# Kernel optimization log

Measured on AMD Instinct MI355X. Metric: run time of the kernel, lower is better.

Reference implementation:

```python
import jax, jax.numpy as jnp
import numpy as np

H_HEADS = 8
HIDDEN = 512
D_K = HIDDEN // H_HEADS


def setup_inputs() -> dict:
    key = jax.random.key(0)
    ks = jax.random.split(key, 16)
    B, T = 4, 1024
    P = 2 * T - 1
    s = 0.02
    inp = {
        "x": jax.random.normal(ks[0], (B, T, HIDDEN), dtype=jnp.float32),
        "pos_emb": jax.random.normal(ks[1], (1, P, HIDDEN), dtype=jnp.float32),
        "Wq": jax.random.normal(ks[2], (HIDDEN, HIDDEN), dtype=jnp.float32) * s,
        "bq": jnp.zeros((HIDDEN,), dtype=jnp.float32),
        "Wk": jax.random.normal(ks[3], (HIDDEN, HIDDEN), dtype=jnp.float32) * s,
        "bk": jnp.zeros((HIDDEN,), dtype=jnp.float32),
        "Wv": jax.random.normal(ks[4], (HIDDEN, HIDDEN), dtype=jnp.float32) * s,
        "bv": jnp.zeros((HIDDEN,), dtype=jnp.float32),
        "Wp": jax.random.normal(ks[5], (HIDDEN, HIDDEN), dtype=jnp.float32) * s,
        "bp": jnp.zeros((HIDDEN,), dtype=jnp.float32),
        "Wo": jax.random.normal(ks[6], (HIDDEN, HIDDEN), dtype=jnp.float32) * s,
        "bo": jnp.zeros((HIDDEN,), dtype=jnp.float32),
        "pos_bias_u": jax.random.normal(ks[7], (H_HEADS, D_K), dtype=jnp.float32) * s,
        "pos_bias_v": jax.random.normal(ks[8], (H_HEADS, D_K), dtype=jnp.float32) * s,
    }
    return inp


def rel_shift(x):
    # x: (B, H, T, P). Transformer-XL relative shift.
    B, H, T, P = x.shape
    x = jnp.pad(x, ((0, 0), (0, 0), (0, 0), (1, 0)))  # (B,H,T,P+1)
    x = x.reshape(B, H, P + 1, T)[:, :, 1:, :]          # drop first row
    return x.reshape(B, H, T, P)


def reference(x, pos_emb, Wq, bq, Wk, bk, Wv, bv, Wp, bp, Wo, bo, pos_bias_u, pos_bias_v):
    B, T, _ = x.shape
    Hh, d = H_HEADS, D_K
    scale = 1.0 / jnp.sqrt(jnp.asarray(d, dtype=x.dtype))

    q = (x @ Wq + bq).reshape(B, T, Hh, d)                       # (B,T,H,d)
    k = (x @ Wk + bk).reshape(B, T, Hh, d).transpose(0, 2, 1, 3)  # (B,H,T,d)
    v = (x @ Wv + bv).reshape(B, T, Hh, d).transpose(0, 2, 1, 3)  # (B,H,T,d)
    P = pos_emb.shape[1]
    p = (pos_emb @ Wp + bp).reshape(pos_emb.shape[0], P, Hh, d).transpose(0, 2, 1, 3)  # (1,H,P,d)

    q_u = (q + pos_bias_u).transpose(0, 2, 1, 3)  # (B,H,T,d)
    q_v = (q + pos_bias_v).transpose(0, 2, 1, 3)  # (B,H,T,d)

    # content-position term with rel-shift (broadcast over batch dim of p)
    matrix_bd = jnp.matmul(q_v, p.transpose(0, 1, 3, 2))  # (B,H,T,P)
    matrix_bd = rel_shift(matrix_bd)[:, :, :, :T] * scale  # (B,H,T,T)

    # content-content term + additive bias, scaled softmax
    scores = jnp.matmul(q_u, k.transpose(0, 1, 3, 2)) * scale + matrix_bd
    attn = jax.nn.softmax(scores.astype(jnp.float32), axis=-1).astype(x.dtype)
    out = jnp.matmul(attn, v)                 # (B,H,T,d)
    out = out.transpose(0, 2, 1, 3).reshape(B, T, Hh * d)
    return out @ Wo + bo
```

## Files before the change

kernel.cpp:

```cpp
#include <hip/hip_runtime.h>
#include <math.h>

#define BATCH 4
#define SEQ   1024
#define HID   512
#define NHEAD 8

typedef unsigned short u16;
typedef unsigned int   u32;
typedef short  short8 __attribute__((ext_vector_type(8)));
typedef float  f32x4  __attribute__((ext_vector_type(4)));

__device__ __forceinline__ u16 f2bf(float x) {
  u32 u = __builtin_bit_cast(u32, x);
  u32 r = (u + 0x7FFFu + ((u >> 16) & 1u)) >> 16;
  return (u16)r;
}

#define DPPMAX(x, ctrl)                                                        \
  x = fmaxf(x, __builtin_bit_cast(float, __builtin_amdgcn_update_dpp(          \
                   0, __builtin_bit_cast(int, x), ctrl, 0xf, 0xf, true)))

__global__ __launch_bounds__(256)
void cvt_two(const float* __restrict__ x, const float* __restrict__ pe,
             u16* __restrict__ xb, u16* __restrict__ peb) {
  int i = blockIdx.x * 256 + threadIdx.x;
  const float* s;
  u16* d;
  if (i < 524288) {
    s = x; d = xb;
  } else {
    i -= 524288;
    if (i >= 262016) return;
    s = pe; d = peb;
  }
  float4 v = *(const float4*)&s[(size_t)i * 4];
  ushort4 o;
  o.x = f2bf(v.x); o.y = f2bf(v.y); o.z = f2bf(v.z); o.w = f2bf(v.w);
  *(ushort4*)&d[(size_t)i * 4] = o;
}

__global__ __launch_bounds__(256)
void transpose_w(const float* w0, const float* w1, const float* w2,
                 const float* w3, const float* w4, u16* __restrict__ wt) {
  const float* src;
  switch (blockIdx.z) {
    case 0: src = w0; break;
    case 1: src = w1; break;
    case 2: src = w2; break;
    case 3: src = w3; break;
    default: src = w4; break;
  }
  u16* dst = wt + (size_t)blockIdx.z * 512 * 512;
  __shared__ float t[32][33];
  const int tx = threadIdx.x, ty = threadIdx.y;
  const int k0 = blockIdx.x * 32, n0 = blockIdx.y * 32;
#pragma unroll
  for (int r = 0; r < 4; ++r)
    t[ty + 8 * r][tx] = src[(size_t)(k0 + ty + 8 * r) * 512 + n0 + tx];
  __syncthreads();
#pragma unroll
  for (int r = 0; r < 4; ++r)
    dst[(size_t)(n0 + ty + 8 * r) * 512 + k0 + tx] = f2bf(t[tx][ty + 8 * r]);
}

template <int MF, int NF>
__device__ __forceinline__ void gemm_core(const u16* __restrict__ A,
                                          const u16* __restrict__ Bt,
                                          int m0, int n0, u16* As, u16* Bs,
                                          f32x4 (&acc)[MF][NF]) {
  const int tid = threadIdx.x;
  const int wid = tid >> 6, lane = tid & 63;
  const int lr = lane & 15, lg = lane >> 4;
  const int wm = wid >> 1, wn = wid & 1;
  const int srow = tid >> 3, sc = tid & 7;
#pragma unroll
  for (int i = 0; i < MF; ++i)
#pragma unroll
    for (int j = 0; j < NF; ++j) acc[i][j] = (f32x4)0.f;

  for (int kt = 0; kt < 8; ++kt) {
    const int k0 = kt * 64;
    short8 la[MF], lb[NF];
#pragma unroll
    for (int r = 0; r < MF; ++r)
      la[r] = *(const short8*)&A[(size_t)(m0 + srow + 32 * r) * 512 + k0 + sc * 8];
#pragma unroll
    for (int r = 0; r < NF; ++r)
      lb[r] = *(const short8*)&Bt[(size_t)(n0 + srow + 32 * r) * 512 + k0 + sc * 8];
    __syncthreads();
#pragma unroll
    for (int r = 0; r < MF; ++r) {
      int row = srow + 32 * r;
      *(short8*)&As[row * 64 + ((sc ^ (row & 7)) * 8)] = la[r];
    }
#pragma unroll
    for (int r = 0; r < NF; ++r) {
      int row = srow + 32 * r;
      *(short8*)&Bs[row * 64 + ((sc ^ (row & 7)) * 8)] = lb[r];
    }
    __syncthreads();
#pragma unroll
    for (int kc = 0; kc < 2; ++kc) {
      const int ch = kc * 4 + lg;
      short8 af[MF], bfr[NF];
#pragma unroll
      for (int mt = 0; mt < MF; ++mt) {
        int row = wm * (MF * 16) + mt * 16 + lr;
        af[mt] = *(const short8*)&As[row * 64 + ((ch ^ (row & 7)) * 8)];
      }
#pragma unroll
      for (int nt = 0; nt < NF; ++nt) {
        int row = wn * (NF * 16) + nt * 16 + lr;
        bfr[nt] = *(const short8*)&Bs[row * 64 + ((ch ^ (row & 7)) * 8)];
      }
#pragma unroll
      for (int mt = 0; mt < MF; ++mt)
#pragma unroll
        for (int nt = 0; nt < NF; ++nt)
          acc[mt][nt] = __builtin_amdgcn_mfma_f32_16x16x32_bf16(
              af[mt], bfr[nt], acc[mt][nt], 0, 0, 0);
    }
  }
}

__global__ __launch_bounds__(256)
void gemm_qkvp(const u16* __restrict__ xbf, const u16* __restrict__ pebf,
               const u16* __restrict__ wt,
               const float* __restrict__ bq, const float* __restrict__ bk,
               const float* __restrict__ bv, const float* __restrict__ bp,
               const float* __restrict__ pbu, const float* __restrict__ pbv,
               u16* __restrict__ qu, u16* __restrict__ qv,
               u16* __restrict__ kk, u16* __restrict__ vt,
               u16* __restrict__ pp) {
  __shared__ __align__(16) u16 As[128 * 64];
  __shared__ __align__(16) u16 Bs[128 * 64];
  const int z = blockIdx.z;
  if (z == 3 && blockIdx.y >= 16) return;
  const u16* A = (z == 3) ? pebf : xbf;
  const u16* Bt = wt + (size_t)z * 512 * 512;
  const float* bias = (z == 0) ? bq : (z == 1) ? bk : (z == 2) ? bv : bp;
  const int m0 = blockIdx.y * 128, n0 = blockIdx.x * 128;

  f32x4 acc[4][4];
  gemm_core<4, 4>(A, Bt, m0, n0, As, Bs, acc);

  const int tid = threadIdx.x, wid = tid >> 6, lane = tid & 63;
  const int lr = lane & 15, lg = lane >> 4, wm = wid >> 1, wn = wid & 1;
#pragma unroll
  for (int mt = 0; mt < 4; ++mt)
#pragma unroll
    for (int nt = 0; nt < 4; ++nt) {
      const int col = n0 + wn * 64 + nt * 16 + lr;
      const int rb = m0 + wm * 64 + mt * 16 + lg * 4;
      const float bcol = bias[col];
      if (z == 0) {
        const float uu = pbu[col], vv = pbv[col];
#pragma unroll
        for (int q = 0; q < 4; ++q) {
          float val = acc[mt][nt][q] + bcol;
          qu[(size_t)(rb + q) * 512 + col] = f2bf(val + uu);
          qv[(size_t)(rb + q) * 512 + col] = f2bf(val + vv);
        }
      } else if (z == 1) {
#pragma unroll
        for (int q = 0; q < 4; ++q)
          kk[(size_t)(rb + q) * 512 + col] = f2bf(acc[mt][nt][q] + bcol);
      } else if (z == 2) {
        ushort4 pk;
        pk.x = f2bf(acc[mt][nt][0] + bcol);
        pk.y = f2bf(acc[mt][nt][1] + bcol);
        pk.z = f2bf(acc[mt][nt][2] + bcol);
        pk.w = f2bf(acc[mt][nt][3] + bcol);
        int bb = rb >> 10, tl = rb & 1023;
        *(ushort4*)&vt[(size_t)((bb * 8 + (col >> 6)) * 64 + (col & 63)) * 1024 + tl] = pk;
      } else {
#pragma unroll
        for (int q = 0; q < 4; ++q)
          if (rb + q < 2047)
            pp[(size_t)(rb + q) * 512 + col] = f2bf(acc[mt][nt][q] + bcol);
      }
    }
}

__global__ __launch_bounds__(256)
void gemm_wo(const u16* __restrict__ ao, const u16* __restrict__ wt,
             const float* __restrict__ bo, float* __restrict__ out) {
  __shared__ __align__(16) u16 As[64 * 64];
  __shared__ __align__(16) u16 Bs[64 * 64];
  const int m0 = blockIdx.y * 64, n0 = blockIdx.x * 64;
  f32x4 acc[2][2];
  gemm_core<2, 2>(ao, wt + (size_t)4 * 512 * 512, m0, n0, As, Bs, acc);
  const int tid = threadIdx.x, wid = tid >> 6, lane = tid & 63;
  const int lr = lane & 15, lg = lane >> 4, wm = wid >> 1, wn = wid & 1;
#pragma unroll
  for (int mt = 0; mt < 2; ++mt)
#pragma unroll
    for (int nt = 0; nt < 2; ++nt) {
      const int col = n0 + wn * 32 + nt * 16 + lr;
      const int rb = m0 + wm * 32 + mt * 16 + lg * 4;
      const float bcol = bo[col];
#pragma unroll
      for (int q = 0; q < 4; ++q)
        out[(size_t)(rb + q) * 512 + col] = acc[mt][nt][q] + bcol;
    }
}

__global__ __launch_bounds__(512)
void attn_mfma(const u16* __restrict__ quP, const u16* __restrict__ qvP,
               const u16* __restrict__ kP, const u16* __restrict__ vtP,
               const u16* __restrict__ pP, u16* __restrict__ ao) {
  __shared__ __align__(16) u16 SM[56832];
  u16* Ps = SM + 16384;

  const int tid = threadIdx.x;
  const int wid = tid >> 6, lane = tid & 63;
  const int lr = lane & 15, lg = lane >> 4;
  const int grp = wid >> 2, wq = wid & 3;
  const int t0 = blockIdx.x * 128, h = blockIdx.y, b = blockIdx.z;
  const int base0 = 896 - t0;

  u16* Ksg = SM + grp * 4096;
  u16* Vsg = SM + 8192 + grp * 4096;
  float* wb = (float*)(SM + 32768) + wid * 1504;
  u16* esw = (u16*)wb;

  short8 aqu[2][2], aqv[2][2];
#pragma unroll
  for (int f = 0; f < 2; ++f)
#pragma unroll
    for (int kc = 0; kc < 2; ++kc) {
      size_t g = (size_t)(b * SEQ + t0 + 32 * wq + 16 * f + lr) * 512 + h * 64 +
                 kc * 32 + lg * 8;
      aqu[f][kc] = *(const short8*)&quP[g];
      aqv[f][kc] = *(const short8*)&qvP[g];
    }
  short8 ones;
#pragma unroll
  for (int i = 0; i < 8; ++i) ones[i] = (short)0x3F80;

  float mrun[2][4];
  f32x4 cL[2], cO[2][4];
#pragma unroll
  for (int f = 0; f < 2; ++f) {
    cL[f] = (f32x4)0.f;
#pragma unroll
    for (int q = 0; q < 4; ++q) mrun[f][q] = -1e30f;
#pragma unroll
    for (int nt = 0; nt < 4; ++nt) cO[f][nt] = (f32x4)0.f;
  }

#pragma unroll
  for (int r = 0; r < 2; ++r) {
    int idx = tid + 512 * r;
    int row = idx >> 3, sc = idx & 7;
    short8 lk = *(const short8*)&kP[(size_t)(b * SEQ + row) * 512 + h * 64 + sc * 8];
    short8 lv = *(const short8*)&vtP[(size_t)((b * 8 + h) * 64 + (row & 63)) * 1024 +
                                     (row >> 6) * 64 + sc * 8];
    *(short8*)&SM[(row >> 6) * 4096 + (row & 63) * 64 + ((sc ^ (row & 7)) * 8)] = lk;
    *(short8*)&SM[8192 + (row >> 6) * 4096 + (row & 63) * 64 + ((sc ^ (row & 7)) * 8)] = lv;
  }
#pragma unroll
  for (int r = 0; r < 4; ++r) {
    int idx = tid + 512 * r;
    int prow = idx >> 3, sc = idx & 7;
    short8 lp = *(const short8*)&pP[(size_t)(base0 + prow) * 512 + h * 64 + sc * 8];
    *(short8*)&Ps[prow * 64 + ((sc ^ (prow & 7)) * 8)] = lp;
  }
  __syncthreads();

  for (int s = 0; s < 8; ++s) {
    short8 nk[2], nv[2], np[2];
    if (s < 7) {
      const int jn = 128 * (s + 1);
#pragma unroll
      for (int r = 0; r < 2; ++r) {
        int idx = tid + 512 * r;
        int row = idx >> 3, sc = idx & 7;
        nk[r] = *(const short8*)&kP[(size_t)(b * SEQ + jn + row) * 512 + h * 64 + sc * 8];
        nv[r] = *(const short8*)&vtP[(size_t)((b * 8 + h) * 64 + (row & 63)) * 1024 +
                                     jn + (row >> 6) * 64 + sc * 8];
        np[r] = *(const short8*)&pP[(size_t)(base0 + 256 + 128 * s + row) * 512 +
                                    h * 64 + sc * 8];
      }
    }

    f32x4 cK[2][4];
#pragma unroll
    for (int f = 0; f < 2; ++f)
#pragma unroll
      for (int nt = 0; nt < 4; ++nt) cK[f][nt] = (f32x4)0.f;
    __builtin_amdgcn_s_setprio(1);
#pragma unroll
    for (int kc = 0; kc < 2; ++kc) {
      const int ch = kc * 4 + lg;
#pragma unroll
      for (int nt = 0; nt < 4; ++nt) {
        int krow = nt * 16 + lr;
        short8 bk = *(const short8*)&Ksg[krow * 64 + ((ch ^ (krow & 7)) * 8)];
        cK[0][nt] = __builtin_amdgcn_mfma_f32_16x16x32_bf16(aqu[0][kc], bk, cK[0][nt], 0, 0, 0);
        cK[1][nt] = __builtin_amdgcn_mfma_f32_16x16x32_bf16(aqu[1][kc], bk, cK[1][nt], 0, 0, 0);
      }
    }
    __builtin_amdgcn_s_setprio(0);

    short8 bvr[2][4];
#pragma unroll
    for (int kc = 0; kc < 2; ++kc) {
      const int ch = kc * 4 + lg;
#pragma unroll
      for (int nt = 0; nt < 4; ++nt) {
        int vr = nt * 16 + lr;
        bvr[kc][nt] = *(const short8*)&Vsg[vr * 64 + ((ch ^ (vr & 7)) * 8)];
      }
    }

#pragma unroll
    for (int f = 0; f < 2; ++f) {
      const int poff = 112 - 32 * wq - 16 * f + 64 * grp + 128 * s;
      f32x4 cP5[5];
#pragma unroll
      for (int i = 0; i < 5; ++i) cP5[i] = (f32x4)0.f;
      __builtin_amdgcn_s_setprio(1);
#pragma unroll
      for (int kc = 0; kc < 2; ++kc) {
        const int ch = kc * 4 + lg;
        const int swz = (ch ^ (lr & 7)) * 8;
#pragma unroll
        for (int pt = 0; pt < 5; ++pt) {
          int pos = (poff + pt * 16 + lr) & 255;
          short8 bp = *(const short8*)&Ps[pos * 64 + swz];
          cP5[pt] = __builtin_amdgcn_mfma_f32_16x16x32_bf16(aqv[f][kc], bp, cP5[pt], 0, 0, 0);
        }
      }
      __builtin_amdgcn_s_setprio(0);

#pragma unroll
      for (int pt = 0; pt < 5; ++pt)
#pragma unroll
        for (int q = 0; q < 4; ++q)
          wb[(lg * 4 + q) * 94 + pt * 16 + lr + lg * 4] = cP5[pt][q];
      float sv[4][4];
#pragma unroll
      for (int nt = 0; nt < 4; ++nt)
#pragma unroll
        for (int q = 0; q < 4; ++q)
          sv[nt][q] = 0.125f * (cK[f][nt][q] +
                                wb[(lg * 4 + q) * 94 + 15 - q + nt * 16 + lr]);

      float pm[4];
#pragma unroll
      for (int q = 0; q < 4; ++q) {
        float tm = fmaxf(fmaxf(sv[0][q], sv[1][q]), fmaxf(sv[2][q], sv[3][q]));
        DPPMAX(tm, 0xB1);
        DPPMAX(tm, 0x4E);
        DPPMAX(tm, 0x141);
        DPPMAX(tm, 0x140);
        pm[q] = tm;
      }
      int need = 0;
#pragma unroll
      for (int q = 0; q < 4; ++q) need |= (pm[q] > mrun[f][q] + 8.f) ? 1 : 0;
      if (__any(need)) {
#pragma unroll
        for (int q = 0; q < 4; ++q) {
          float mnew = fmaxf(mrun[f][q], pm[q]);
          float corr = __expf(mrun[f][q] - mnew);
          mrun[f][q] = mnew;
          cL[f][q] *= corr;
#pragma unroll
          for (int nt = 0; nt < 4; ++nt) cO[f][nt][q] *= corr;
        }
      }

#pragma unroll
      for (int nt = 0; nt < 4; ++nt) {
        int jp = nt * 16 + lr, sw = jp >> 3, jb8 = jp & 7;
#pragma unroll
        for (int q = 0; q < 4; ++q) {
          int m = lg * 4 + q;
          esw[m * 64 + ((sw ^ (m & 7)) * 8) + jb8] = f2bf(__expf(sv[nt][q] - mrun[f][q]));
        }
      }

      __builtin_amdgcn_s_setprio(1);
#pragma unroll
      for (int kc = 0; kc < 2; ++kc) {
        const int ch = kc * 4 + lg;
        short8 ae = *(const short8*)&esw[lr * 64 + ((ch ^ (lr & 7)) * 8)];
        cL[f] = __builtin_amdgcn_mfma_f32_16x16x32_bf16(ae, ones, cL[f], 0, 0, 0);
#pragma unroll
        for (int nt = 0; nt < 4; ++nt)
          cO[f][nt] = __builtin_amdgcn_mfma_f32_16x16x32_bf16(ae, bvr[kc][nt], cO[f][nt], 0, 0, 0);
      }
      __builtin_amdgcn_s_setprio(0);
    }

    __syncthreads();
    if (s < 7) {
#pragma unroll
      for (int r = 0; r < 2; ++r) {
        int idx = tid + 512 * r;
        int row = idx >> 3, sc = idx & 7;
        *(short8*)&SM[(row >> 6) * 4096 + (row & 63) * 64 + ((sc ^ (row & 7)) * 8)] = nk[r];
        *(short8*)&SM[8192 + (row >> 6) * 4096 + (row & 63) * 64 + ((sc ^ (row & 7)) * 8)] = nv[r];
        int pos = (128 * s + row) & 255;
        *(short8*)&Ps[pos * 64 + ((sc ^ (pos & 7)) * 8)] = np[r];
      }
    }
    __syncthreads();
  }

  float* ob = (float*)SM;
  float* mlb = (float*)(SM + 16384);
  if (grp == 1) {
#pragma unroll
    for (int f = 0; f < 2; ++f) {
#pragma unroll
      for (int nt = 0; nt < 4; ++nt)
#pragma unroll
        for (int q = 0; q < 4; ++q)
          ob[(wq * 32 + 16 * f + 4 * lg + q) * 64 + nt * 16 + lr] = cO[f][nt][q];
      if (lr == 0) {
#pragma unroll
        for (int q = 0; q < 4; ++q) {
          int rr = wq * 32 + 16 * f + 4 * lg + q;
          mlb[rr * 2 + 0] = mrun[f][q];
          mlb[rr * 2 + 1] = cL[f][q];
        }
      }
    }
  }
  __syncthreads();
  if (grp == 0) {
#pragma unroll
    for (int f = 0; f < 2; ++f) {
      float ws0[4], ws1[4];
#pragma unroll
      for (int q = 0; q < 4; ++q) {
        int rr = wq * 32 + 16 * f + 4 * lg + q;
        float m1 = mlb[rr * 2 + 0], l1 = mlb[rr * 2 + 1];
        float M = fmaxf(mrun[f][q], m1);
        float w0 = __expf(mrun[f][q] - M), w1 = __expf(m1 - M);
        float inv = 1.f / (w0 * cL[f][q] + w1 * l1);
        ws0[q] = w0 * inv;
        ws1[q] = w1 * inv;
      }
#pragma unroll
      for (int nt = 0; nt < 4; ++nt)
#pragma unroll
        for (int q = 0; q < 4; ++q) {
          int rr = wq * 32 + 16 * f + 4 * lg + q;
          float o1 = ob[rr * 64 + nt * 16 + lr];
          float val = ws0[q] * cO[f][nt][q] + ws1[q] * o1;
          ao[(size_t)(b * SEQ + t0 + rr) * 512 + h * 64 + nt * 16 + lr] = f2bf(val);
        }
    }
  }
}

extern "C" void kernel_launch(void* const* d_in, const int* in_sizes, int n_in,
                              void* d_out, int out_size, void* d_ws, size_t ws_size,
                              hipStream_t stream) {
  const float* x   = (const float*)d_in[0];
  const float* pe  = (const float*)d_in[1];
  const float* Wq  = (const float*)d_in[2];
  const float* bq  = (const float*)d_in[3];
  const float* Wk  = (const float*)d_in[4];
  const float* bk  = (const float*)d_in[5];
  const float* Wv  = (const float*)d_in[6];
  const float* bv  = (const float*)d_in[7];
  const float* Wp  = (const float*)d_in[8];
  const float* bp  = (const float*)d_in[9];
  const float* Wo  = (const float*)d_in[10];
  const float* bo  = (const float*)d_in[11];
  const float* pbu = (const float*)d_in[12];
  const float* pbv = (const float*)d_in[13];

  char* ws = (char*)d_ws;
  size_t o = 0;
  auto alloc = [&](size_t bytes) { size_t r = o; o += (bytes + 255) & ~(size_t)255; return r; };
  u16* x_bf  = (u16*)(ws + alloc((size_t)4096 * 512 * 2));
  u16* pe_bf = (u16*)(ws + alloc((size_t)2048 * 512 * 2));
  u16* wt    = (u16*)(ws + alloc((size_t)5 * 512 * 512 * 2));
  u16* qu    = (u16*)(ws + alloc((size_t)4096 * 512 * 2));
  u16* qv    = (u16*)(ws + alloc((size_t)4096 * 512 * 2));
  u16* kk    = (u16*)(ws + alloc((size_t)4096 * 512 * 2));
  u16* vt    = (u16*)(ws + alloc((size_t)4096 * 512 * 2));
  u16* pp    = (u16*)(ws + alloc((size_t)2048 * 512 * 2));
  u16* ao    = (u16*)(ws + alloc((size_t)4096 * 512 * 2));

  dim3 blk(256);
  cvt_two<<<dim3(3072), blk, 0, stream>>>(x, pe, x_bf, pe_bf);
  transpose_w<<<dim3(16, 16, 5), dim3(32, 8), 0, stream>>>(Wq, Wk, Wv, Wp, Wo, wt);
  hipMemsetAsync(pp + (size_t)2047 * 512, 0, 512 * 2, stream);

  gemm_qkvp<<<dim3(4, 32, 4), blk, 0, stream>>>(x_bf, pe_bf, wt, bq, bk, bv, bp,
                                                pbu, pbv, qu, qv, kk, vt, pp);
  attn_mfma<<<dim3(8, NHEAD, BATCH), dim3(512), 0, stream>>>(qu, qv, kk, vt, pp, ao);
  gemm_wo<<<dim3(8, 64), blk, 0, stream>>>(ao, wt, bo, (float*)d_out);
}
```

Baseline: 82.78 us.

## Compute transposed score tiles so each lane owns one query row

Swaps the MFMA operand order for the QK and QP products, so the accumulators come out transposed and each lane holds one query row across four key columns. The row max now needs only two cross-lane shuffles instead of a four-step DPP reduction per element. The rel-shift staging buffer is written with vector stores, and the bf16 probabilities are packed and stored as 64-bit words instead of scalar 16-bit stores. In exchange, the rescale factors and final running maxima have to be broadcast back to the original accumulator layout with shuffles, and the shifted LDS read pattern changes, which may alter bank conflicts.

```diff
diff --git a/kernel.cpp b/kernel.cpp
--- a/kernel.cpp
+++ b/kernel.cpp
@@ -16,10 +16,6 @@
   u32 r = (u + 0x7FFFu + ((u >> 16) & 1u)) >> 16;
   return (u16)r;
 }
-
-#define DPPMAX(x, ctrl)                                                        \
-  x = fmaxf(x, __builtin_bit_cast(float, __builtin_amdgcn_update_dpp(          \
-                   0, __builtin_bit_cast(int, x), ctrl, 0xf, 0xf, true)))
 
 __global__ __launch_bounds__(256)
 void cvt_two(const float* __restrict__ x, const float* __restrict__ pe,
@@ -222,8 +218,8 @@
 
   u16* Ksg = SM + grp * 4096;
   u16* Vsg = SM + 8192 + grp * 4096;
-  float* wb = (float*)(SM + 32768) + wid * 1504;
-  u16* esw = (u16*)wb;
+  float* wbf = (float*)(SM + 32768) + wid * 1504;
+  u16* esw = (u16*)wbf;
 
   short8 aqu[2][2], aqv[2][2];
 #pragma unroll
@@ -239,13 +235,11 @@
 #pragma unroll
   for (int i = 0; i < 8; ++i) ones[i] = (short)0x3F80;
 
-  float mrun[2][4];
+  float mrun[2] = {-1e30f, -1e30f};
   f32x4 cL[2], cO[2][4];
 #pragma unroll
   for (int f = 0; f < 2; ++f) {
     cL[f] = (f32x4)0.f;
-#pragma unroll
-    for (int q = 0; q < 4; ++q) mrun[f][q] = -1e30f;
 #pragma unroll
     for (int nt = 0; nt < 4; ++nt) cO[f][nt] = (f32x4)0.f;
   }
@@ -285,11 +279,11 @@
       }
     }
 
-    f32x4 cK[2][4];
+    f32x4 cKT[2][4];
 #pragma unroll
     for (int f = 0; f < 2; ++f)
 #pragma unroll
-      for (int nt = 0; nt < 4; ++nt) cK[f][nt] = (f32x4)0.f;
+      for (int nt = 0; nt < 4; ++nt) cKT[f][nt] = (f32x4)0.f;
     __builtin_amdgcn_s_setprio(1);
 #pragma unroll
     for (int kc = 0; kc < 2; ++kc) {
@@ -298,8 +292,8 @@
       for (int nt = 0; nt < 4; ++nt) {
         int krow = nt * 16 + lr;
         short8 bk = *(const short8*)&Ksg[krow * 64 + ((ch ^ (krow & 7)) * 8)];
-        cK[0][nt] = __builtin_amdgcn_mfma_f32_16x16x32_bf16(aqu[0][kc], bk, cK[0][nt], 0, 0, 0);
-        cK[1][nt] = __builtin_amdgcn_mfma_f32_16x16x32_bf16(aqu[1][kc], bk, cK[1][nt], 0, 0, 0);
+        cKT[0][nt] = __builtin_amdgcn_mfma_f32_16x16x32_bf16(bk, aqu[0][kc], cKT[0][nt], 0, 0, 0);
+        cKT[1][nt] = __builtin_amdgcn_mfma_f32_16x16x32_bf16(bk, aqu[1][kc], cKT[1][nt], 0, 0, 0);
       }
     }
     __builtin_amdgcn_s_setprio(0);
@@ -318,9 +312,9 @@
 #pragma unroll
     for (int f = 0; f < 2; ++f) {
       const int poff = 112 - 32 * wq - 16 * f + 64 * grp + 128 * s;
-      f32x4 cP5[5];
-#pragma unroll
-      for (int i = 0; i < 5; ++i) cP5[i] = (f32x4)0.f;
+      f32x4 cPT[5];
+#pragma unroll
+      for (int i = 0; i < 5; ++i) cPT[i] = (f32x4)0.f;
       __builtin_amdgcn_s_setprio(1);
 #pragma unroll
       for (int kc = 0; kc < 2; ++kc) {
@@ -330,68 +324,67 @@
         for (int pt = 0; pt < 5; ++pt) {
           int pos = (poff + pt * 16 + lr) & 255;
           short8 bp = *(const short8*)&Ps[pos * 64 + swz];
-          cP5[pt] = __builtin_amdgcn_mfma_f32_16x16x32_bf16(aqv[f][kc], bp, cP5[pt], 0, 0, 0);
+          cPT[pt] = __builtin_amdgcn_mfma_f32_16x16x32_bf16(bp, aqv[f][kc], cPT[pt], 0, 0, 0);
         }
       }
       __builtin_amdgcn_s_setprio(0);
 
 #pragma unroll
       for (int pt = 0; pt < 5; ++pt)
+        *(f32x4*)&wbf[lr * 84 + pt * 16 + lg * 4] = cPT[pt];
+      float sv[4][4];
+#pragma unroll
+      for (int nt = 0; nt < 4; ++nt)
 #pragma unroll
         for (int q = 0; q < 4; ++q)
-          wb[(lg * 4 + q) * 94 + pt * 16 + lr + lg * 4] = cP5[pt][q];
-      float sv[4][4];
+          sv[nt][q] = 0.125f * (cKT[f][nt][q] +
+                                wbf[lr * 84 + 16 * nt + lg * 4 + q + 15 - lr]);
+
+      float tm = sv[0][0];
 #pragma unroll
       for (int nt = 0; nt < 4; ++nt)
 #pragma unroll
+        for (int q = 0; q < 4; ++q) tm = fmaxf(tm, sv[nt][q]);
+      tm = fmaxf(tm, __shfl_xor(tm, 16));
+      tm = fmaxf(tm, __shfl_xor(tm, 32));
+      if (__any(tm > mrun[f] + 8.f)) {
+        float mnew = fmaxf(mrun[f], tm);
+        float corr = __expf(mrun[f] - mnew);
+        mrun[f] = mnew;
+        float cc[4];
+#pragma unroll
         for (int q = 0; q < 4; ++q)
-          sv[nt][q] = 0.125f * (cK[f][nt][q] +
-                                wb[(lg * 4 + q) * 94 + 15 - q + nt * 16 + lr]);
-
-      float pm[4];
-#pragma unroll
-      for (int q = 0; q < 4; ++q) {
-        float tm = fmaxf(fmaxf(sv[0][q], sv[1][q]), fmaxf(sv[2][q], sv[3][q]));
-        DPPMAX(tm, 0xB1);
-        DPPMAX(tm, 0x4E);
-        DPPMAX(tm, 0x141);
-        DPPMAX(tm, 0x140);
-        pm[q] = tm;
-      }
-      int need = 0;
-#pragma unroll
-      for (int q = 0; q < 4; ++q) need |= (pm[q] > mrun[f][q] + 8.f) ? 1 : 0;
-      if (__any(need)) {
+          cc[q] = __shfl(corr, (lane & 48) | (lg * 4 + q));
 #pragma unroll
         for (int q = 0; q < 4; ++q) {
-          float mnew = fmaxf(mrun[f][q], pm[q]);
-          float corr = __expf(mrun[f][q] - mnew);
-          mrun[f][q] = mnew;
-          cL[f][q] *= corr;
-#pragma unroll
-          for (int nt = 0; nt < 4; ++nt) cO[f][nt][q] *= corr;
+          cL[f][q] *= cc[q];
+#pragma unroll
+          for (int nt = 0; nt < 4; ++nt) cO[f][nt][q] *= cc[q];
         }
       }
 
 #pragma unroll
       for (int nt = 0; nt < 4; ++nt) {
-        int jp = nt * 16 + lr, sw = jp >> 3, jb8 = jp & 7;
-#pragma unroll
-        for (int q = 0; q < 4; ++q) {
-          int m = lg * 4 + q;
-          esw[m * 64 + ((sw ^ (m & 7)) * 8) + jb8] = f2bf(__expf(sv[nt][q] - mrun[f][q]));
-        }
+        float e0 = __expf(sv[nt][0] - mrun[f]);
+        float e1 = __expf(sv[nt][1] - mrun[f]);
+        float e2 = __expf(sv[nt][2] - mrun[f]);
+        float e3 = __expf(sv[nt][3] - mrun[f]);
+        uint2 pk;
+        pk.x = (u32)f2bf(e0) | ((u32)f2bf(e1) << 16);
+        pk.y = (u32)f2bf(e2) | ((u32)f2bf(e3) << 16);
+        int g = 2 * nt + (lg >> 1);
+        *(uint2*)&esw[lr * 64 + ((g ^ (lr & 7)) * 8) + (lg & 1) * 4] = pk;
       }
 
       __builtin_amdgcn_s_setprio(1);
 #pragma unroll
       for (int kc = 0; kc < 2; ++kc) {
         const int ch = kc * 4 + lg;
-        short8 ae = *(const short8*)&esw[lr * 64 + ((ch ^ (lr & 7)) * 8)];
-        cL[f] = __builtin_amdgcn_mfma_f32_16x16x32_bf16(ae, ones, cL[f], 0, 0, 0);
+        short8 pa = *(const short8*)&esw[lr * 64 + ((ch ^ (lr & 7)) * 8)];
+        cL[f] = __builtin_amdgcn_mfma_f32_16x16x32_bf16(pa, ones, cL[f], 0, 0, 0);
 #pragma unroll
         for (int nt = 0; nt < 4; ++nt)
-          cO[f][nt] = __builtin_amdgcn_mfma_f32_16x16x32_bf16(ae, bvr[kc][nt], cO[f][nt], 0, 0, 0);
+          cO[f][nt] = __builtin_amdgcn_mfma_f32_16x16x32_bf16(pa, bvr[kc][nt], cO[f][nt], 0, 0, 0);
       }
       __builtin_amdgcn_s_setprio(0);
     }
@@ -411,6 +404,13 @@
     __syncthreads();
   }
 
+  float m_c[2][4];
+#pragma unroll
+  for (int f = 0; f < 2; ++f)
+#pragma unroll
+    for (int q = 0; q < 4; ++q)
+      m_c[f][q] = __shfl(mrun[f], (lane & 48) | (lg * 4 + q));
+
   float* ob = (float*)SM;
   float* mlb = (float*)(SM + 16384);
   if (grp == 1) {
@@ -425,7 +425,7 @@
 #pragma unroll
         for (int q = 0; q < 4; ++q) {
           int rr = wq * 32 + 16 * f + 4 * lg + q;
-          mlb[rr * 2 + 0] = mrun[f][q];
+          mlb[rr * 2 + 0] = m_c[f][q];
           mlb[rr * 2 + 1] = cL[f][q];
         }
       }
@@ -440,8 +440,8 @@
       for (int q = 0; q < 4; ++q) {
         int rr = wq * 32 + 16 * f + 4 * lg + q;
         float m1 = mlb[rr * 2 + 0], l1 = mlb[rr * 2 + 1];
-        float M = fmaxf(mrun[f][q], m1);
-        float w0 = __expf(mrun[f][q] - M), w1 = __expf(m1 - M);
+        float M = fmaxf(m_c[f][q], m1);
+        float w0 = __expf(m_c[f][q] - M), w1 = __expf(m1 - M);
         float inv = 1.f / (w0 * cL[f][q] + w1 * l1);
         ws0[q] = w0 * inv;
         ws1[q] = w1 * inv;
```

Result: faster. 76.82 us (median of 2 runs) (-7.2%).
